# Optimization experiments

Hardware: AMD Instinct MI355X
Metric: run time of the kernel (lower is better)

Reference implementation:

```python
import jax, jax.numpy as jnp
import numpy as np

B, S, D = 2, 2048, 2048
HQ, HKV, HD = 16, 4, 128
EPS = 1e-8


def _rope_tables(seq_len, dim, base=10000.0):
    inv_freq = 1.0 / (base ** (jnp.arange(0, dim, 2, dtype=jnp.float32) / dim))
    freqs = jnp.outer(jnp.arange(seq_len, dtype=jnp.float32), inv_freq)  # S x dim/2
    emb = jnp.concatenate([freqs, freqs], axis=-1)  # S x dim
    return jnp.cos(emb), jnp.sin(emb)


def setup_inputs() -> dict:
    key = jax.random.key(0)
    ks = jax.random.split(key, 6)
    cos_theta, sin_theta = _rope_tables(S, HD)
    return {
        "x": jax.random.normal(ks[0], (B, S, D), dtype=jnp.float32),
        "Wq": jax.random.normal(ks[1], (D, HQ * HD), dtype=jnp.float32) * 0.02,
        "Wk": jax.random.normal(ks[2], (D, HKV * HD), dtype=jnp.float32) * 0.02,
        "Wv": jax.random.normal(ks[3], (D, HKV * HD), dtype=jnp.float32) * 0.02,
        "Wo": jax.random.normal(ks[4], (HQ * HD, D), dtype=jnp.float32) * 0.02,
        "q_norm_w": jnp.zeros((HD,), dtype=jnp.float32),
        "k_norm_w": jnp.zeros((HD,), dtype=jnp.float32),
        "cos_theta": cos_theta,
        "sin_theta": sin_theta,
        "padding_mask": jnp.zeros((B, S), dtype=bool),
        "window_size": 1024,
    }


def _rmsnorm(x, w):
    return x * jax.lax.rsqrt(jnp.mean(x * x, axis=-1, keepdims=True) + EPS) * (1.0 + w)


def _rotate_half(x):
    x1, x2 = jnp.split(x, 2, axis=-1)
    return jnp.concatenate([-x2, x1], axis=-1)


def _rope(x, cos_t, sin_t):
    # x: B x H x S x d; cos/sin: S x d
    return x * cos_t[None, None] + _rotate_half(x) * sin_t[None, None]


def reference(x, Wq, Wk, Wv, Wo, q_norm_w, k_norm_w, cos_theta, sin_theta, padding_mask, window_size):
    b, s, _ = x.shape
    scale = HD ** -0.5
    q = (x @ Wq).reshape(b, s, HQ, HD).transpose(0, 2, 1, 3)   # b,HQ,s,d
    k = (x @ Wk).reshape(b, s, HKV, HD).transpose(0, 2, 1, 3)  # b,HKV,s,d
    v = (x @ Wv).reshape(b, s, HKV, HD).transpose(0, 2, 1, 3)
    q = _rope(_rmsnorm(q, q_norm_w), cos_theta[:s], sin_theta[:s])
    k = _rope(_rmsnorm(k, k_norm_w), cos_theta[:s], sin_theta[:s])

    # causal & sliding window & padding mask
    qi = jnp.arange(s)[:, None]
    ki = jnp.arange(s)[None, :]
    mask = (qi >= ki) & ((qi - ki) <= window_size)          # s x s
    pad = padding_mask[:, :, None] | padding_mask[:, None, :]  # b x s x s
    mask = mask[None] & ~pad                                 # b x s x s

    g = HQ // HKV
    qg = q.reshape(b, HKV, g, s, HD)
    scores = jnp.einsum('bngqd,bnkd->bngqk', qg, k) * scale  # b,HKV,g,s,s
    scores = jnp.where(mask[:, None, None], scores, -jnp.inf)
    attn = jax.nn.softmax(scores, axis=-1)
    out = jnp.einsum('bngqk,bnkd->bngqd', attn, v)
    out = out.reshape(b, HQ, s, HD).transpose(0, 2, 1, 3).reshape(b, s, HQ * HD)
    return out @ Wo
```

## Files before the change

### kernel.cpp

```cpp
#include <hip/hip_runtime.h>

typedef __attribute__((ext_vector_type(4))) float f32x4;
typedef __attribute__((ext_vector_type(8))) __bf16 bf16x8;
typedef __attribute__((ext_vector_type(4))) __bf16 bf16x4;

__device__ __forceinline__ void gload_lds16(const __bf16* g, __bf16* l) {
  __builtin_amdgcn_global_load_lds(
      (const __attribute__((address_space(1))) unsigned int*)(g),
      (__attribute__((address_space(3))) unsigned int*)(l), 16, 0, 0);
}

__global__ __launch_bounds__(256) void prep(
    const float* __restrict__ Wq, const float* __restrict__ Wk,
    const float* __restrict__ Wv, const float* __restrict__ Wo,
    const float4* __restrict__ x, const unsigned long long* __restrict__ pad,
    __bf16* __restrict__ Wqkvt, __bf16* __restrict__ Wot,
    bf16x4* __restrict__ xb, unsigned char* __restrict__ pad64) {
  const int bx = blockIdx.x, by = blockIdx.y;
  const int tx = threadIdx.x, ty = threadIdx.y;
  const int tid = ty * 32 + tx;
  if (bx >= 160) {
    int i = ((bx - 160) * 64 + by) * 256 + tid;
    float4 v = x[i];
    bf16x4 o = {(__bf16)v.x, (__bf16)v.y, (__bf16)v.z, (__bf16)v.w};
    xb[i] = o;
    return;
  }
  if (bx == 0 && by == 0 && tid < 64) {
    unsigned long long acc = 0;
#pragma unroll
    for (int i = 0; i < 8; ++i) acc |= pad[tid * 8 + i];
    pad64[tid] = (acc != 0) ? 1 : 0;
  }
  __shared__ float t[32][33];
  const float* src; __bf16* dst; int ss, c0;
  if (bx < 64)      { src = Wq; dst = Wqkvt;                       ss = 2048; c0 = bx * 32; }
  else if (bx < 80) { src = Wk; dst = Wqkvt + (size_t)2048 * 2048; ss = 512;  c0 = (bx - 64) * 32; }
  else if (bx < 96) { src = Wv; dst = Wqkvt + (size_t)2560 * 2048; ss = 512;  c0 = (bx - 80) * 32; }
  else              { src = Wo; dst = Wot;                         ss = 2048; c0 = (bx - 96) * 32; }
  const int r0 = by * 32;
#pragma unroll
  for (int i = ty; i < 32; i += 8)
    t[i][tx] = src[(size_t)(r0 + i) * ss + c0 + tx];
  __syncthreads();
#pragma unroll
  for (int i = ty; i < 32; i += 8)
    dst[(size_t)(c0 + i) * 2048 + r0 + tx] = (__bf16)t[tx][i];
}

__device__ __forceinline__ void stage5(const __bf16* aS, const __bf16* bS,
                                       __bf16* Ab, __bf16* Bb, int wb8, size_t kt) {
#pragma unroll
  for (int l = 0; l < 2; ++l)
    gload_lds16(aS + (size_t)l * 131072 + kt, Ab + l * 4096 + wb8);
#pragma unroll
  for (int l = 0; l < 3; ++l)
    gload_lds16(bS + (size_t)l * 131072 + kt, Bb + l * 4096 + wb8);
}

__global__ __launch_bounds__(512, 4) void gemm_qkv192(
    const __bf16* __restrict__ A, const __bf16* __restrict__ Bt,
    __bf16* __restrict__ Qb, __bf16* __restrict__ Kb, __bf16* __restrict__ Vt) {
  extern __shared__ __bf16 smem[];
  const int K = 2048;
  const int tid = threadIdx.x;
  const int lane = tid & 63, w = tid >> 6;
  const int c15 = lane & 15, quad = lane >> 4;
  const int wm = w >> 2, wn = w & 3;
  const int id = blockIdx.x;
  const int swz = (id & 7) * 64 + (id >> 3);
  const int m0 = (swz >> 4) * 128, n0 = (swz & 15) * 192;

  const int srow = tid >> 3;
  const int scol = ((tid & 7) ^ (srow & 7)) * 8;
  const __bf16* aSrc = A + (size_t)(m0 + srow) * K + scol;
  const __bf16* bSrc = Bt + (size_t)(n0 + srow) * K + scol;
  const int wb8 = (tid & 448) * 8;
  f32x4 acc[4][3] = {};

  stage5(aSrc, bSrc, smem, smem + 8192, wb8, 0);
  stage5(aSrc, bSrc, smem + 20480, smem + 28672, wb8, 64);

  for (int t = 0; t < 32; ++t) {
    __bf16* Ab = smem + (t & 1) * 20480;
    __bf16* Bb = Ab + 8192;
    if (t < 31) asm volatile("s_waitcnt vmcnt(5)" ::: "memory");
    else        asm volatile("s_waitcnt vmcnt(0)" ::: "memory");
    __builtin_amdgcn_s_barrier();
    __builtin_amdgcn_sched_barrier(0);

    bf16x8 bF[3][2];
#pragma unroll
    for (int j = 0; j < 3; ++j) {
      int RB = wn * 48 + j * 16 + c15;
#pragma unroll
      for (int h = 0; h < 2; ++h)
        bF[j][h] = *(const bf16x8*)(Bb + RB * 64 + (((h * 4 + quad) ^ (RB & 7)) * 8));
    }
    __builtin_amdgcn_s_setprio(1);
#pragma unroll
    for (int i = 0; i < 4; ++i) {
      int RA = wm * 64 + i * 16 + c15;
      bf16x8 a0 = *(const bf16x8*)(Ab + RA * 64 + ((quad ^ (RA & 7)) * 8));
      bf16x8 a1 = *(const bf16x8*)(Ab + RA * 64 + (((4 + quad) ^ (RA & 7)) * 8));
#pragma unroll
      for (int j = 0; j < 3; ++j) {
        acc[i][j] = __builtin_amdgcn_mfma_f32_16x16x32_bf16(a0, bF[j][0], acc[i][j], 0, 0, 0);
        acc[i][j] = __builtin_amdgcn_mfma_f32_16x16x32_bf16(a1, bF[j][1], acc[i][j], 0, 0, 0);
      }
    }
    __builtin_amdgcn_s_setprio(0);
    __builtin_amdgcn_sched_barrier(0);
    asm volatile("s_waitcnt lgkmcnt(0)" ::: "memory");
    __builtin_amdgcn_s_barrier();
    __builtin_amdgcn_sched_barrier(0);
    if (t < 30) stage5(aSrc, bSrc, Ab, Bb, wb8, (size_t)(t + 2) * 64);
  }

  const int b = m0 >> 11;
  const int s0 = m0 & 2047;
  const int colbase = n0 + wn * 48;
  __bf16* st = smem + w * 5120;

#pragma unroll
  for (int i = 0; i < 4; ++i)
#pragma unroll
    for (int j = 0; j < 3; ++j)
#pragma unroll
      for (int r = 0; r < 4; ++r)
        st[(i * 16 + quad * 4 + r) * 56 + j * 16 + c15] = (__bf16)acc[i][j][r];
  __syncthreads();

  {
    const int g = lane & 7, sl = lane >> 3;
    int c = colbase + g * 8;
    if (g < 6 && c < 2560) {
      __bf16* hp = (c < 2048)
          ? Qb + (((size_t)b * 16 + (c >> 7)) * 2048 + s0 + wm * 64) * 128 + (c & 127)
          : Kb + (((size_t)b * 4 + ((c - 2048) >> 7)) * 2048 + s0 + wm * 64) * 128 + (c & 127);
#pragma unroll
      for (int it = 0; it < 8; ++it) {
        int s = it * 8 + sl;
        *(bf16x8*)(hp + (size_t)s * 128) = *(const bf16x8*)(st + s * 56 + g * 8);
      }
    }
  }
#pragma unroll
  for (int it = 0; it < 6; ++it) {
    int lc = it * 8 + (lane >> 3);
    int c = colbase + lc;
    if (c >= 2560) {
      int sc = lane & 7;
      bf16x8 o;
#pragma unroll
      for (int rr = 0; rr < 8; ++rr) o[rr] = st[(sc * 8 + rr) * 56 + lc];
      __bf16* vp = Vt + (((size_t)b * 4 + ((c - 2560) >> 7)) * 128 + ((c - 2560) & 127)) * 2048
                   + s0 + wm * 64 + sc * 8;
      *(bf16x8*)vp = o;
    }
  }
}

__global__ __launch_bounds__(256) void norm_rope(
    __bf16* __restrict__ Qb, __bf16* __restrict__ Kb,
    const float* __restrict__ qw, const float* __restrict__ kw,
    const float* __restrict__ cosT, const float* __restrict__ sinT) {
  const int tid = threadIdx.x, w = tid >> 6, lane = tid & 63;
  const int v = blockIdx.x * 4 + w;
  const bool isQ = v < 65536;
  __bf16* base = isQ ? Qb + (size_t)v * 128 : Kb + (size_t)(v - 65536) * 128;
  const int s = v & 2047;
  float x1 = (float)base[lane], x2 = (float)base[lane + 64];
  float ss = x1 * x1 + x2 * x2;
#pragma unroll
  for (int d = 32; d; d >>= 1) ss += __shfl_xor(ss, d);
  float rn = rsqrtf(ss * (1.0f / 128.0f) + 1e-8f);
  const float* wt = isQ ? qw : kw;
  float n1 = x1 * rn * (1.0f + wt[lane]);
  float n2 = x2 * rn * (1.0f + wt[lane + 64]);
  float c1 = cosT[s * 128 + lane], c2 = cosT[s * 128 + 64 + lane];
  float s1 = sinT[s * 128 + lane], s2 = sinT[s * 128 + 64 + lane];
  const float QSC = 0.08838834764831845f * 1.4426950408889634f;
  float post = isQ ? QSC : 1.0f;
  base[lane]      = (__bf16)((n1 * c1 - n2 * s1) * post);
  base[lane + 64] = (__bf16)((n2 * c2 + n1 * s2) * post);
}

__global__ __launch_bounds__(256) void gemm_bt(const __bf16* __restrict__ A,
                                               const __bf16* __restrict__ Bt,
                                               float* __restrict__ C,
                                               int M, int N, int K) {
  __shared__ __align__(16) __bf16 As[128 * 32];
  __shared__ __align__(16) __bf16 Bs[128 * 32];
  const int tid = threadIdx.x;
  const int lane = tid & 63;
  const int c15 = lane & 15, quad = lane >> 4;
  const int wm = ((tid >> 6) & 1) * 64;
  const int wn = (tid >> 7) * 64;
  const int m0 = blockIdx.y * 128, n0 = blockIdx.x * 128;
  const int wbase = tid & 192;

  f32x4 acc[4][4] = {};

  const int row0 = tid >> 2, cc0 = (tid & 3) * 8;
  const int row1 = (tid + 256) >> 2;
  const __bf16* a0 = A + (size_t)(m0 + row0) * K + cc0;
  const __bf16* a1 = A + (size_t)(m0 + row1) * K + cc0;
  const __bf16* b0 = Bt + (size_t)(n0 + row0) * K + cc0;
  const __bf16* b1 = Bt + (size_t)(n0 + row1) * K + cc0;
  __bf16* lA0 = As + (size_t)wbase * 8;
  __bf16* lA1 = As + (size_t)(256 + wbase) * 8;
  __bf16* lB0 = Bs + (size_t)wbase * 8;
  __bf16* lB1 = Bs + (size_t)(256 + wbase) * 8;

  for (int k0 = 0; k0 < K; k0 += 32) {
    gload_lds16(a0 + k0, lA0);
    gload_lds16(a1 + k0, lA1);
    gload_lds16(b0 + k0, lB0);
    gload_lds16(b1 + k0, lB1);
    __syncthreads();
    bf16x8 af[4], bfr[4];
#pragma unroll
    for (int i = 0; i < 4; ++i) {
      af[i]  = *(const bf16x8*)(As + (wm + i * 16 + c15) * 32 + quad * 8);
      bfr[i] = *(const bf16x8*)(Bs + (wn + i * 16 + c15) * 32 + quad * 8);
    }
#pragma unroll
    for (int i = 0; i < 4; ++i)
#pragma unroll
      for (int j = 0; j < 4; ++j)
        acc[i][j] = __builtin_amdgcn_mfma_f32_16x16x32_bf16(af[i], bfr[j], acc[i][j], 0, 0, 0);
    __syncthreads();
  }

#pragma unroll
  for (int i = 0; i < 4; ++i) {
    int r0 = m0 + wm + i * 16 + quad * 4;
#pragma unroll
    for (int j = 0; j < 4; ++j) {
      int cc = n0 + wn + j * 16 + c15;
#pragma unroll
      for (int r = 0; r < 4; ++r)
        C[(size_t)(r0 + r) * N + cc] = acc[i][j][r];
    }
  }
}

__global__ __launch_bounds__(256) void attn(
    const __bf16* __restrict__ Qb, const __bf16* __restrict__ Kb,
    const __bf16* __restrict__ Vt, const unsigned char* __restrict__ pad,
    const unsigned char* __restrict__ pad64, const int* __restrict__ winp,
    __bf16* __restrict__ O) {
  const int S = 2048;
  __shared__ __align__(16) __bf16 Ks[64 * 128];
  __shared__ __align__(16) __bf16 Vs[128 * 64];
  __shared__ __align__(16) __bf16 Ps[4 * 32 * 72];
  const int tid = threadIdx.x, w = tid >> 6, lane = tid & 63;
  const int c15 = lane & 15, quad = lane >> 4;
  const int b = blockIdx.z;
  const int bx = (b == 0) ? blockIdx.x : (gridDim.x - 1 - blockIdx.x);
  const int q0 = ((int)gridDim.x - 1 - bx) * 32;
  const int kv = blockIdx.y;
  const int h = kv * 4 + w;
  const int W = *winp;
  const unsigned char* padb = pad + (size_t)b * S;
  const unsigned char* pad64b = pad64 + b * 32;
  const __bf16* Qh = Qb + (((size_t)b * 16 + h) * S) * 128;
  const __bf16* Kh = Kb + (((size_t)b * 4 + kv) * S) * 128;
  const __bf16* Vh = Vt + (((size_t)b * 4 + kv) * 128) * (size_t)S;
  __bf16* Pw = Ps + w * 32 * 72;

  bf16x8 qf0[4], qf1[4];
#pragma unroll
  for (int c = 0; c < 4; ++c) {
    qf0[c] = *(const bf16x8*)(Qh + (size_t)(q0 + c15) * 128 + c * 32 + quad * 8);
    qf1[c] = *(const bf16x8*)(Qh + (size_t)(q0 + 16 + c15) * 128 + c * 32 + quad * 8);
  }

  f32x4 acc0[8] = {}, acc1[8] = {};
  float lsum0[4] = {0.f, 0.f, 0.f, 0.f};
  float lsum1[4] = {0.f, 0.f, 0.f, 0.f};

  const int krow_i = lane >> 4, kch = lane & 15;
  const int vrow_i = lane >> 3, vch = lane & 7;

  int kb0 = q0 - W; if (kb0 < 0) kb0 = 0; kb0 &= ~63;

  for (int kb = kb0; kb <= q0 + 31; kb += 64) {
    __syncthreads();
#pragma unroll
    for (int i = 0; i < 4; ++i) {
      int row = w * 16 + i * 4 + krow_i;
      gload_lds16(Kh + (size_t)(kb + row) * 128 + ((kch ^ (row & 15)) * 8),
                  Ks + (w * 16 + i * 4) * 128);
    }
#pragma unroll
    for (int i = 0; i < 4; ++i) {
      int row = w * 32 + i * 8 + vrow_i;
      gload_lds16(Vh + (size_t)row * S + kb + ((vch ^ (row & 7)) * 8),
                  Vs + (w * 32 + i * 8) * 64);
    }
    __syncthreads();

    f32x4 sf0[4], sf1[4];
#pragma unroll
    for (int nb = 0; nb < 4; ++nb) {
      f32x4 ca = {}, cb = {};
#pragma unroll
      for (int c = 0; c < 4; ++c) {
        bf16x8 kf = *(const bf16x8*)(Ks + (nb * 16 + c15) * 128 + (((c * 4 + quad) ^ c15) * 8));
        ca = __builtin_amdgcn_mfma_f32_16x16x32_bf16(qf0[c], kf, ca, 0, 0, 0);
        cb = __builtin_amdgcn_mfma_f32_16x16x32_bf16(qf1[c], kf, cb, 0, 0, 0);
      }
      sf0[nb] = ca; sf1[nb] = cb;
    }

    const bool fast = (kb + 63 <= q0) && (q0 + 31 - kb <= W) && (pad64b[kb >> 6] == 0);
    if (fast) {
#pragma unroll
      for (int r = 0; r < 4; ++r) {
        float a0 = exp2f(sf0[0][r]), a1 = exp2f(sf0[1][r]);
        float a2 = exp2f(sf0[2][r]), a3 = exp2f(sf0[3][r]);
        lsum0[r] += (a0 + a1) + (a2 + a3);
        int pr = (quad * 4 + r) * 72 + c15;
        Pw[pr] = (__bf16)a0; Pw[pr + 16] = (__bf16)a1;
        Pw[pr + 32] = (__bf16)a2; Pw[pr + 48] = (__bf16)a3;
        float b0 = exp2f(sf1[0][r]), b1 = exp2f(sf1[1][r]);
        float b2 = exp2f(sf1[2][r]), b3 = exp2f(sf1[3][r]);
        lsum1[r] += (b0 + b1) + (b2 + b3);
        int qr = pr + 16 * 72;
        Pw[qr] = (__bf16)b0; Pw[qr + 16] = (__bf16)b1;
        Pw[qr + 32] = (__bf16)b2; Pw[qr + 48] = (__bf16)b3;
      }
    } else {
#pragma unroll
      for (int r = 0; r < 4; ++r) {
        const int qi0 = q0 + quad * 4 + r;
        const int qi1 = qi0 + 16;
        float p0[4], p1[4];
#pragma unroll
        for (int nb = 0; nb < 4; ++nb) {
          int ki = kb + nb * 16 + c15;
          bool okp = (padb[ki] == 0);
          bool ok0 = (ki <= qi0) && ((qi0 - ki) <= W) && okp;
          bool ok1 = (ki <= qi1) && ((qi1 - ki) <= W) && okp;
          float e0 = exp2f(sf0[nb][r]);
          float e1 = exp2f(sf1[nb][r]);
          p0[nb] = ok0 ? e0 : 0.0f;
          p1[nb] = ok1 ? e1 : 0.0f;
        }
        lsum0[r] += (p0[0] + p0[1]) + (p0[2] + p0[3]);
        lsum1[r] += (p1[0] + p1[1]) + (p1[2] + p1[3]);
        int pr = (quad * 4 + r) * 72 + c15;
        Pw[pr] = (__bf16)p0[0]; Pw[pr + 16] = (__bf16)p0[1];
        Pw[pr + 32] = (__bf16)p0[2]; Pw[pr + 48] = (__bf16)p0[3];
        int qr = pr + 16 * 72;
        Pw[qr] = (__bf16)p1[0]; Pw[qr + 16] = (__bf16)p1[1];
        Pw[qr + 32] = (__bf16)p1[2]; Pw[qr + 48] = (__bf16)p1[3];
      }
    }

    bf16x8 pf00 = *(const bf16x8*)(Pw + c15 * 72 + quad * 8);
    bf16x8 pf01 = *(const bf16x8*)(Pw + c15 * 72 + 32 + quad * 8);
    bf16x8 pf10 = *(const bf16x8*)(Pw + (16 + c15) * 72 + quad * 8);
    bf16x8 pf11 = *(const bf16x8*)(Pw + (16 + c15) * 72 + 32 + quad * 8);
#pragma unroll
    for (int nb = 0; nb < 8; ++nb) {
      int row = nb * 16 + c15;
      bf16x8 vf0 = *(const bf16x8*)(Vs + row * 64 + ((quad ^ (c15 & 7)) * 8));
      bf16x8 vf1 = *(const bf16x8*)(Vs + row * 64 + (((4 + quad) ^ (c15 & 7)) * 8));
      acc0[nb] = __builtin_amdgcn_mfma_f32_16x16x32_bf16(pf00, vf0, acc0[nb], 0, 0, 0);
      acc0[nb] = __builtin_amdgcn_mfma_f32_16x16x32_bf16(pf01, vf1, acc0[nb], 0, 0, 0);
      acc1[nb] = __builtin_amdgcn_mfma_f32_16x16x32_bf16(pf10, vf0, acc1[nb], 0, 0, 0);
      acc1[nb] = __builtin_amdgcn_mfma_f32_16x16x32_bf16(pf11, vf1, acc1[nb], 0, 0, 0);
    }
  }

#pragma unroll
  for (int r = 0; r < 4; ++r) {
    lsum0[r] += __shfl_xor(lsum0[r], 1);
    lsum0[r] += __shfl_xor(lsum0[r], 2);
    lsum0[r] += __shfl_xor(lsum0[r], 4);
    lsum0[r] += __shfl_xor(lsum0[r], 8);
    lsum1[r] += __shfl_xor(lsum1[r], 1);
    lsum1[r] += __shfl_xor(lsum1[r], 2);
    lsum1[r] += __shfl_xor(lsum1[r], 4);
    lsum1[r] += __shfl_xor(lsum1[r], 8);
  }
  float inv0[4], inv1[4];
#pragma unroll
  for (int r = 0; r < 4; ++r) { inv0[r] = 1.0f / lsum0[r]; inv1[r] = 1.0f / lsum1[r]; }
#pragma unroll
  for (int nb = 0; nb < 8; ++nb)
#pragma unroll
    for (int r = 0; r < 4; ++r) {
      size_t idx = ((size_t)b * S + q0 + quad * 4 + r) * 2048 + h * 128 + nb * 16 + c15;
      O[idx] = (__bf16)(acc0[nb][r] * inv0[r]);
      O[idx + (size_t)16 * 2048] = (__bf16)(acc1[nb][r] * inv1[r]);
    }
}

extern "C" void kernel_launch(void* const* d_in, const int* in_sizes, int n_in,
                              void* d_out, int out_size, void* d_ws, size_t ws_size,
                              hipStream_t stream) {
  const float* x    = (const float*)d_in[0];
  const float* Wq   = (const float*)d_in[1];
  const float* Wk   = (const float*)d_in[2];
  const float* Wv   = (const float*)d_in[3];
  const float* Wo   = (const float*)d_in[4];
  const float* qw   = (const float*)d_in[5];
  const float* kw   = (const float*)d_in[6];
  const float* cosT = (const float*)d_in[7];
  const float* sinT = (const float*)d_in[8];
  const unsigned char* pad = (const unsigned char*)d_in[9];
  const int* win    = (const int*)d_in[10];

  char* ws = (char*)d_ws;
  __bf16* xb    = (__bf16*)(ws + 0);
  __bf16* Wqkvt = (__bf16*)(ws + 16777216);
  __bf16* Wot   = (__bf16*)(ws + 29360128);
  __bf16* Qb    = (__bf16*)(ws + 37748736);
  __bf16* Kb    = (__bf16*)(ws + 54525952);
  __bf16* Vt    = (__bf16*)(ws + 58720256);
  __bf16* Ob    = (__bf16*)(ws + 62914560);
  unsigned char* pad64 = (unsigned char*)(ws + 79691776);

  static int qkv_attr = (int)hipFuncSetAttribute(
      (const void*)gemm_qkv192, hipFuncAttributeMaxDynamicSharedMemorySize, 81920);
  (void)qkv_attr;

  prep<<<dim3(288, 64, 1), dim3(32, 8, 1), 0, stream>>>(
      Wq, Wk, Wv, Wo, (const float4*)x, (const unsigned long long*)pad,
      Wqkvt, Wot, (bf16x4*)xb, pad64);

  gemm_qkv192<<<dim3(512, 1, 1), 512, 81920, stream>>>(xb, Wqkvt, Qb, Kb, Vt);

  norm_rope<<<20480, 256, 0, stream>>>(Qb, Kb, qw, kw, cosT, sinT);

  attn<<<dim3(64, 4, 2), 256, 0, stream>>>(Qb, Kb, Vt, pad, pad64, win, Ob);

  gemm_bt<<<dim3(16, 32, 1), 256, 0, stream>>>(Ob, Wot, (float*)d_out, 4096, 2048, 2048);
}
```

Measured before the change: 320.5 us.

## Replace output GEMM with double-buffered 512-thread kernel and simplify QKV pipeline

The output projection GEMM is rewritten as a 512-thread, 128x128-tile kernel. It uses 64-wide K steps, XOR-swizzled LDS, double buffering with direct global-to-LDS loads, and block-id swizzling. This replaces the single-buffered 32-wide-K version, aiming to overlap loads with MFMA work and cut LDS bank conflicts. The QKV GEMM pipeline is reworked from a two-stage prefetch with explicit vmcnt waits into a one-ahead prefetch with __syncthreads. That is simpler but may hide less memory latency there.

```diff
diff --git a/kernel.cpp b/kernel.cpp
--- a/kernel.cpp
+++ b/kernel.cpp
@@ -79,16 +79,15 @@
   f32x4 acc[4][3] = {};
 
   stage5(aSrc, bSrc, smem, smem + 8192, wb8, 0);
-  stage5(aSrc, bSrc, smem + 20480, smem + 28672, wb8, 64);
+  __syncthreads();
 
   for (int t = 0; t < 32; ++t) {
     __bf16* Ab = smem + (t & 1) * 20480;
     __bf16* Bb = Ab + 8192;
-    if (t < 31) asm volatile("s_waitcnt vmcnt(5)" ::: "memory");
-    else        asm volatile("s_waitcnt vmcnt(0)" ::: "memory");
-    __builtin_amdgcn_s_barrier();
-    __builtin_amdgcn_sched_barrier(0);
-
+    if (t < 31) {
+      __bf16* An = smem + ((t + 1) & 1) * 20480;
+      stage5(aSrc, bSrc, An, An + 8192, wb8, (size_t)(t + 1) * 64);
+    }
     bf16x8 bF[3][2];
 #pragma unroll
     for (int j = 0; j < 3; ++j) {
@@ -110,11 +109,7 @@
       }
     }
     __builtin_amdgcn_s_setprio(0);
-    __builtin_amdgcn_sched_barrier(0);
-    asm volatile("s_waitcnt lgkmcnt(0)" ::: "memory");
-    __builtin_amdgcn_s_barrier();
-    __builtin_amdgcn_sched_barrier(0);
-    if (t < 30) stage5(aSrc, bSrc, Ab, Bb, wb8, (size_t)(t + 2) * 64);
+    __syncthreads();
   }
 
   const int b = m0 >> 11;
@@ -186,59 +181,77 @@
   base[lane + 64] = (__bf16)((n2 * c2 + n1 * s2) * post);
 }
 
-__global__ __launch_bounds__(256) void gemm_bt(const __bf16* __restrict__ A,
-                                               const __bf16* __restrict__ Bt,
-                                               float* __restrict__ C,
-                                               int M, int N, int K) {
-  __shared__ __align__(16) __bf16 As[128 * 32];
-  __shared__ __align__(16) __bf16 Bs[128 * 32];
+__device__ __forceinline__ void stage4(const __bf16* aS, const __bf16* bS,
+                                       __bf16* Ab, __bf16* Bb, int wb8, size_t kt) {
+#pragma unroll
+  for (int l = 0; l < 2; ++l)
+    gload_lds16(aS + (size_t)l * 131072 + kt, Ab + l * 4096 + wb8);
+#pragma unroll
+  for (int l = 0; l < 2; ++l)
+    gload_lds16(bS + (size_t)l * 131072 + kt, Bb + l * 4096 + wb8);
+}
+
+__global__ __launch_bounds__(512, 4) void gemm_bt128(
+    const __bf16* __restrict__ A, const __bf16* __restrict__ Bt,
+    float* __restrict__ C) {
+  extern __shared__ __bf16 smem[];
+  const int K = 2048, N = 2048;
   const int tid = threadIdx.x;
-  const int lane = tid & 63;
+  const int lane = tid & 63, w = tid >> 6;
   const int c15 = lane & 15, quad = lane >> 4;
-  const int wm = ((tid >> 6) & 1) * 64;
-  const int wn = (tid >> 7) * 64;
-  const int m0 = blockIdx.y * 128, n0 = blockIdx.x * 128;
-  const int wbase = tid & 192;
-
-  f32x4 acc[4][4] = {};
-
-  const int row0 = tid >> 2, cc0 = (tid & 3) * 8;
-  const int row1 = (tid + 256) >> 2;
-  const __bf16* a0 = A + (size_t)(m0 + row0) * K + cc0;
-  const __bf16* a1 = A + (size_t)(m0 + row1) * K + cc0;
-  const __bf16* b0 = Bt + (size_t)(n0 + row0) * K + cc0;
-  const __bf16* b1 = Bt + (size_t)(n0 + row1) * K + cc0;
-  __bf16* lA0 = As + (size_t)wbase * 8;
-  __bf16* lA1 = As + (size_t)(256 + wbase) * 8;
-  __bf16* lB0 = Bs + (size_t)wbase * 8;
-  __bf16* lB1 = Bs + (size_t)(256 + wbase) * 8;
-
-  for (int k0 = 0; k0 < K; k0 += 32) {
-    gload_lds16(a0 + k0, lA0);
-    gload_lds16(a1 + k0, lA1);
-    gload_lds16(b0 + k0, lB0);
-    gload_lds16(b1 + k0, lB1);
+  const int wm = w >> 2, wn = w & 3;
+  const int id = blockIdx.x;
+  const int swz = (id & 7) * 64 + (id >> 3);
+  const int m0 = (swz >> 4) * 128, n0 = (swz & 15) * 128;
+
+  const int srow = tid >> 3;
+  const int scol = ((tid & 7) ^ (srow & 7)) * 8;
+  const __bf16* aSrc = A + (size_t)(m0 + srow) * K + scol;
+  const __bf16* bSrc = Bt + (size_t)(n0 + srow) * K + scol;
+  const int wb8 = (tid & 448) * 8;
+
+  f32x4 acc[4][2] = {};
+
+  stage4(aSrc, bSrc, smem, smem + 8192, wb8, 0);
+  __syncthreads();
+
+  for (int t = 0; t < 32; ++t) {
+    __bf16* Ab = smem + (t & 1) * 16384;
+    __bf16* Bb = Ab + 8192;
+    if (t < 31) {
+      __bf16* An = smem + ((t + 1) & 1) * 16384;
+      stage4(aSrc, bSrc, An, An + 8192, wb8, (size_t)(t + 1) * 64);
+    }
+    bf16x8 bF[2][2];
+#pragma unroll
+    for (int j = 0; j < 2; ++j) {
+      int RB = wn * 32 + j * 16 + c15;
+#pragma unroll
+      for (int h = 0; h < 2; ++h)
+        bF[j][h] = *(const bf16x8*)(Bb + RB * 64 + (((h * 4 + quad) ^ (RB & 7)) * 8));
+    }
+    __builtin_amdgcn_s_setprio(1);
+#pragma unroll
+    for (int i = 0; i < 4; ++i) {
+      int RA = wm * 64 + i * 16 + c15;
+      bf16x8 a0 = *(const bf16x8*)(Ab + RA * 64 + ((quad ^ (RA & 7)) * 8));
+      bf16x8 a1 = *(const bf16x8*)(Ab + RA * 64 + (((4 + quad) ^ (RA & 7)) * 8));
+#pragma unroll
+      for (int j = 0; j < 2; ++j) {
+        acc[i][j] = __builtin_amdgcn_mfma_f32_16x16x32_bf16(a0, bF[j][0], acc[i][j], 0, 0, 0);
+        acc[i][j] = __builtin_amdgcn_mfma_f32_16x16x32_bf16(a1, bF[j][1], acc[i][j], 0, 0, 0);
+      }
+    }
+    __builtin_amdgcn_s_setprio(0);
     __syncthreads();
-    bf16x8 af[4], bfr[4];
-#pragma unroll
-    for (int i = 0; i < 4; ++i) {
-      af[i]  = *(const bf16x8*)(As + (wm + i * 16 + c15) * 32 + quad * 8);
-      bfr[i] = *(const bf16x8*)(Bs + (wn + i * 16 + c15) * 32 + quad * 8);
-    }
-#pragma unroll
-    for (int i = 0; i < 4; ++i)
-#pragma unroll
-      for (int j = 0; j < 4; ++j)
-        acc[i][j] = __builtin_amdgcn_mfma_f32_16x16x32_bf16(af[i], bfr[j], acc[i][j], 0, 0, 0);
-    __syncthreads();
   }
 
 #pragma unroll
   for (int i = 0; i < 4; ++i) {
-    int r0 = m0 + wm + i * 16 + quad * 4;
-#pragma unroll
-    for (int j = 0; j < 4; ++j) {
-      int cc = n0 + wn + j * 16 + c15;
+    int r0 = m0 + wm * 64 + i * 16 + quad * 4;
+#pragma unroll
+    for (int j = 0; j < 2; ++j) {
+      int cc = n0 + wn * 32 + j * 16 + c15;
 #pragma unroll
       for (int r = 0; r < 4; ++r)
         C[(size_t)(r0 + r) * N + cc] = acc[i][j][r];
@@ -428,6 +441,9 @@
   static int qkv_attr = (int)hipFuncSetAttribute(
       (const void*)gemm_qkv192, hipFuncAttributeMaxDynamicSharedMemorySize, 81920);
   (void)qkv_attr;
+  static int bt_attr = (int)hipFuncSetAttribute(
+      (const void*)gemm_bt128, hipFuncAttributeMaxDynamicSharedMemorySize, 65536);
+  (void)bt_attr;
 
   prep<<<dim3(288, 64, 1), dim3(32, 8, 1), 0, stream>>>(
       Wq, Wk, Wv, Wo, (const float4*)x, (const unsigned long long*)pad,
@@ -439,5 +455,5 @@
 
   attn<<<dim3(64, 4, 2), 256, 0, stream>>>(Qb, Kb, Vt, pad, pad64, win, Ob);
 
-  gemm_bt<<<dim3(16, 32, 1), 256, 0, stream>>>(Ob, Wot, (float*)d_out, 4096, 2048, 2048);
-}
+  gemm_bt128<<<dim3(512, 1, 1), 512, 65536, stream>>>(Ob, Wot, (float*)d_out);
+}
```

Result: faster. 305.7 us (-4.6%).
